# Optimization experiments

Hardware: AMD Instinct MI355X
Metric: run time of the kernel (lower is better)

Reference implementation:

```python
import jax, jax.numpy as jnp
import numpy as np

N = 100000
E = 1600000
IN_C, HID_C, OUT_C = 64, 64, 40
EPS = 1e-5


def setup_inputs() -> dict:
    key = jax.random.key(0)
    ks = jax.random.split(key, 16)
    x = jax.random.normal(ks[0], (N, IN_C), dtype=jnp.float32)
    edge_index = jax.random.randint(ks[1], (2, E), 0, N, dtype=jnp.int64)

    def glorot(k, fan_in, fan_out):
        s = jnp.sqrt(6.0 / (fan_in + fan_out)).astype(jnp.float32)
        return jax.random.uniform(k, (fan_in, fan_out), jnp.float32, -s, s)

    return {
        "x": x,
        "edge_index": edge_index,
        # layer 0: SAGEConv(IN_C -> HID_C): out = mean_aggr @ Wl + x @ Wr + b
        "Wl0": glorot(ks[2], IN_C, HID_C), "Wr0": glorot(ks[3], IN_C, HID_C),
        "b0": jnp.zeros((HID_C,), jnp.float32),
        # layer 1: SAGEConv(HID_C -> HID_C)
        "Wl1": glorot(ks[4], HID_C, HID_C), "Wr1": glorot(ks[5], HID_C, HID_C),
        "b1": jnp.zeros((HID_C,), jnp.float32),
        # layer 2: SAGEConv(HID_C -> OUT_C)
        "Wl2": glorot(ks[6], HID_C, OUT_C), "Wr2": glorot(ks[7], HID_C, OUT_C),
        "b2": jnp.zeros((OUT_C,), jnp.float32),
        # batch norms after layers 0 and 1
        "g0": jnp.ones((HID_C,), jnp.float32), "be0": jnp.zeros((HID_C,), jnp.float32),
        "g1": jnp.ones((HID_C,), jnp.float32), "be1": jnp.zeros((HID_C,), jnp.float32),
    }


def _sage_conv(x, src, dst, Wl, Wr, b):
    # mean aggregation of source features at destination nodes (PyG SAGEConv, aggr='mean')
    agg = jax.ops.segment_sum(x[src], dst, num_segments=N)  # [N, C]
    deg = jax.ops.segment_sum(jnp.ones((src.shape[0],), x.dtype), dst, num_segments=N)
    mean = agg / jnp.maximum(deg, 1.0)[:, None]
    return mean @ Wl + x @ Wr + b


def _batch_norm(x, gamma, beta):
    mu = jnp.mean(x, axis=0)
    var = jnp.var(x, axis=0)
    return (x - mu) * jax.lax.rsqrt(var + EPS) * gamma + beta


def reference(x, edge_index, Wl0, Wr0, b0, Wl1, Wr1, b1, Wl2, Wr2, b2, g0, be0, g1, be1):
    src, dst = edge_index[0], edge_index[1]
    h = _sage_conv(x, src, dst, Wl0, Wr0, b0)
    h = jax.nn.relu(_batch_norm(h, g0, be0))  # dropout is identity at inference
    h = _sage_conv(h, src, dst, Wl1, Wr1, b1)
    h = jax.nn.relu(_batch_norm(h, g1, be1))
    return _sage_conv(h, src, dst, Wl2, Wr2, b2)
```

## Files before the change

### kernel.cpp

```cpp
#include <hip/hip_runtime.h>


constexpr float BN_EPS = 1e-5f;

typedef __attribute__((ext_vector_type(8))) short bf16x8;
typedef __attribute__((ext_vector_type(4))) float f32x4;

__device__ __forceinline__ float bf2f(unsigned short u) {
  union { unsigned int i; float f; } c;
  c.i = (unsigned int)u << 16;
  return c.f;
}
__device__ __forceinline__ unsigned short f2bf(float v) {
  union { float f; unsigned int i; } c;
  c.f = v;
  unsigned int r = c.i + 0x7fffu + ((c.i >> 16) & 1u);
  return (unsigned short)(r >> 16);
}

__device__ __forceinline__ float ld_f(const float* p, size_t i) { return p[i]; }
__device__ __forceinline__ float ld_f(const unsigned short* p, size_t i) {
  return bf2f(p[i]);
}
__device__ __forceinline__ void st_f(float* p, size_t i, float v) { p[i] = v; }
__device__ __forceinline__ void st_f(unsigned short* p, size_t i, float v) {
  p[i] = f2bf(v);
}

__device__ __forceinline__ float4 ld_row(const float* p, int row, int li) {
  return ((const float4*)p)[(size_t)row * 16 + li];
}
__device__ __forceinline__ float4 ld_row(const unsigned short* p, int row, int li) {
  ushort4 u = ((const ushort4*)p)[(size_t)row * 16 + li];
  float4 f;
  f.x = bf2f(u.x); f.y = bf2f(u.y); f.z = bf2f(u.z); f.w = bf2f(u.w);
  return f;
}

__global__ __launch_bounds__(256) void k_zero(int* __restrict__ p, int n) {
  int i = blockIdx.x * 256 + threadIdx.x;
  if (i < n) p[i] = 0;
}

__global__ __launch_bounds__(256) void k_probe(const int* __restrict__ w, int E,
                                               int* __restrict__ dflag) {
  __shared__ int any;
  if (threadIdx.x == 0) any = 0;
  __syncthreads();
  const int twoE = 2 * E;
  int local = 0;
  for (int i = 0; i < 8; ++i) {
    long long idx = (long long)(threadIdx.x * 8 + i) * twoE / 2048;
    int wi = (int)(idx | 1);
    if (wi < twoE && w[wi] != 0) local = 1;
  }
  if (local) atomicOr(&any, 1);
  __syncthreads();
  if (threadIdx.x == 0) *dflag = any;
}

__device__ __forceinline__ void load_edge(const void* ei, int e, int E, int is32,
                                          int& src, int& dst) {
  if (is32) {
    const int* p = (const int*)ei;
    src = p[e];
    dst = p[E + e];
  } else {
    const long long* p = (const long long*)ei;
    src = (int)p[e];
    dst = (int)p[(long long)E + e];
  }
}

__global__ __launch_bounds__(256) void k_hist(const void* __restrict__ ei, int E,
                                              int N, const int* __restrict__ dflag,
                                              int NB, int chunk,
                                              int* __restrict__ hist) {
  __shared__ int h[256];
  h[threadIdx.x] = 0;
  __syncthreads();
  const int is32 = *dflag;
  int lo = blockIdx.x * chunk;
  int hi = lo + chunk;
  if (hi > E) hi = E;
  for (int e = lo + threadIdx.x; e < hi; e += 256) {
    int src, dst;
    load_edge(ei, e, E, is32, src, dst);
    if ((unsigned)src < (unsigned)N && (unsigned)dst < (unsigned)N)
      atomicAdd(&h[dst >> 9], 1);
  }
  __syncthreads();
  if (threadIdx.x < NB) hist[blockIdx.x * NB + threadIdx.x] = h[threadIdx.x];
}

__global__ __launch_bounds__(256) void k_btot(const int* __restrict__ hist,
                                              int NBLK, int NB,
                                              int* __restrict__ bucket_base) {
  __shared__ int part[256];
  int t = threadIdx.x;
  int s = 0;
  if (t < NB)
    for (int b = 0; b < NBLK; ++b) s += hist[b * NB + t];
  part[t] = s;
  __syncthreads();
  for (int off = 1; off < 256; off <<= 1) {
    int u = (t >= off) ? part[t - off] : 0;
    __syncthreads();
    part[t] += u;
    __syncthreads();
  }
  if (t < NB) bucket_base[t] = part[t] - s;
  if (t == NB - 1) bucket_base[NB] = part[t];
}

__global__ __launch_bounds__(64) void k_hoff(const int* __restrict__ hist,
                                             int NBLK, int NB,
                                             const int* __restrict__ bucket_base,
                                             int* __restrict__ offs) {
  int b = blockIdx.x;
  int lane = threadIdx.x;
  int carry = bucket_base[b];
  for (int c = 0; c < NBLK; c += 64) {
    int blk = c + lane;
    int v = (blk < NBLK) ? hist[blk * NB + b] : 0;
    int incl = v;
    for (int off = 1; off < 64; off <<= 1) {
      int u = __shfl_up(incl, off);
      if (lane >= off) incl += u;
    }
    if (blk < NBLK) offs[blk * NB + b] = carry + incl - v;
    carry += __shfl(incl, 63);
  }
}

__global__ __launch_bounds__(256) void k_scat(const void* __restrict__ ei, int E,
                                              int N, const int* __restrict__ dflag,
                                              int NB, int chunk,
                                              const int* __restrict__ offs,
                                              unsigned* __restrict__ csr) {
  __shared__ int cur[256];
  if (threadIdx.x < NB) cur[threadIdx.x] = offs[blockIdx.x * NB + threadIdx.x];
  __syncthreads();
  const int is32 = *dflag;
  int lo = blockIdx.x * chunk;
  int hi = lo + chunk;
  if (hi > E) hi = E;
  for (int e = lo + threadIdx.x; e < hi; e += 256) {
    int src, dst;
    load_edge(ei, e, E, is32, src, dst);
    if ((unsigned)src < (unsigned)N && (unsigned)dst < (unsigned)N) {
      int p = atomicAdd(&cur[dst >> 9], 1);
      csr[p] = ((unsigned)src << 9) | (unsigned)(dst & 511);
    }
  }
}

__global__ __launch_bounds__(256) void k_fine(unsigned* __restrict__ csr,
                                              const int* __restrict__ bucket_base,
                                              int N, int* __restrict__ row_start) {
  constexpr int CAP = 12288;
  __shared__ unsigned lrec[CAP];
  __shared__ int lcnt[512];
  __shared__ int cur[512];
  __shared__ int wtot[4];
  const int b = blockIdx.x;
  const int lo = bucket_base[b];
  int cnt = bucket_base[b + 1] - lo;
  if (cnt > CAP) cnt = CAP;
  const int t = threadIdx.x;
  lcnt[t] = 0;
  lcnt[t + 256] = 0;
  __syncthreads();
  for (int i = t; i < cnt; i += 256) {
    unsigned r = csr[lo + i];
    lrec[i] = r;
    atomicAdd(&lcnt[r & 511], 1);
  }
  __syncthreads();
  int v0 = lcnt[2 * t], v1 = lcnt[2 * t + 1];
  int s = v0 + v1;
  int incl = s;
  const int lane = t & 63;
  for (int off = 1; off < 64; off <<= 1) {
    int u = __shfl_up(incl, off);
    if (lane >= off) incl += u;
  }
  const int wv = t >> 6;
  if (lane == 63) wtot[wv] = incl;
  __syncthreads();
  int woff = 0;
  for (int i = 0; i < wv; ++i) woff += wtot[i];
  int excl = woff + incl - s;
  cur[2 * t] = excl;
  cur[2 * t + 1] = excl + v0;
  int gi = b * 512 + 2 * t;
  if (gi <= N) row_start[gi] = lo + excl;
  if (gi + 1 <= N) row_start[gi + 1] = lo + excl + v0;
  __syncthreads();
  for (int i = t; i < cnt; i += 256) {
    unsigned r = lrec[i];
    int p = atomicAdd(&cur[r & 511], 1);
    csr[lo + p] = r >> 9;
  }
}

template <int COUT, typename TI, typename TO>
__global__ __launch_bounds__(256, 4) void k_sage(
    const TI* __restrict__ hin, const int* __restrict__ row_start,
    const int* __restrict__ csr, const float* __restrict__ Wl,
    const float* __restrict__ Wr, const float* __restrict__ bias,
    TO* __restrict__ out, int n) {
  constexpr int NT = (COUT + 15) / 16;
  __shared__ short sWf[NT][4][64][8];
  __shared__ short sA[4][16][136];

  for (int t = threadIdx.x; t < NT * 4 * 64; t += 256) {
    int lane = t & 63;
    int kt = (t >> 6) & 3;
    int nt = t >> 8;
    int kbase = kt * 32 + (lane >> 4) * 8;
    int col = nt * 16 + (lane & 15);
#pragma unroll
    for (int j = 0; j < 8; ++j) {
      int k = kbase + j;
      float wv = 0.0f;
      if (col < COUT) wv = (k < 64) ? Wl[k * COUT + col] : Wr[(k - 64) * COUT + col];
      sWf[nt][kt][lane][j] = (short)f2bf(wv);
    }
  }
  __syncthreads();

  const int wave = threadIdx.x >> 6;
  const int lane = threadIdx.x & 63;
  const int g = lane >> 4;
  const int li = lane & 15;
  const int quad = lane >> 4;
  const int col16 = lane & 15;

  float bias_r[NT];
#pragma unroll
  for (int nt = 0; nt < NT; ++nt) {
    int c = nt * 16 + col16;
    bias_r[nt] = (c < COUT) ? bias[c] : 0.0f;
  }

  const int wgl = blockIdx.x * 4 + wave;
  const int nstride = gridDim.x * 64;

  for (int base = wgl * 16; base < n; base += nstride) {
#pragma unroll 1
    for (int nb = 0; nb < 16; ++nb) {
      int node = base + nb;
      if (node >= n) break;
      int rs = row_start[node];
      int re = row_start[node + 1];
      float4 acc = make_float4(0.f, 0.f, 0.f, 0.f);
      int e = rs + g;
      for (; e + 4 < re; e += 8) {
        int r0 = csr[e], r1 = csr[e + 4];
        float4 a = ld_row(hin, r0, li);
        float4 b = ld_row(hin, r1, li);
        acc.x += a.x + b.x;
        acc.y += a.y + b.y;
        acc.z += a.z + b.z;
        acc.w += a.w + b.w;
      }
      if (e < re) {
        float4 a = ld_row(hin, csr[e], li);
        acc.x += a.x; acc.y += a.y; acc.z += a.z; acc.w += a.w;
      }
      acc.x += __shfl_xor(acc.x, 16); acc.x += __shfl_xor(acc.x, 32);
      acc.y += __shfl_xor(acc.y, 16); acc.y += __shfl_xor(acc.y, 32);
      acc.z += __shfl_xor(acc.z, 16); acc.z += __shfl_xor(acc.z, 32);
      acc.w += __shfl_xor(acc.w, 16); acc.w += __shfl_xor(acc.w, 32);
      int deg = re - rs;
      float invd = 1.0f / (float)(deg > 0 ? deg : 1);
      float4 self = ld_row(hin, node, li);
      ushort4 mv, sv;
      mv.x = f2bf(acc.x * invd); mv.y = f2bf(acc.y * invd);
      mv.z = f2bf(acc.z * invd); mv.w = f2bf(acc.w * invd);
      sv.x = f2bf(self.x); sv.y = f2bf(self.y);
      sv.z = f2bf(self.z); sv.w = f2bf(self.w);
      *(ushort4*)&sA[wave][nb][li * 4] = mv;
      *(ushort4*)&sA[wave][nb][64 + li * 4] = sv;
    }
    __builtin_amdgcn_wave_barrier();

    f32x4 acc[NT];
#pragma unroll
    for (int nt = 0; nt < NT; ++nt) acc[nt] = (f32x4){0.f, 0.f, 0.f, 0.f};
#pragma unroll
    for (int kt = 0; kt < 4; ++kt) {
      bf16x8 a = *(const bf16x8*)&sA[wave][lane & 15][kt * 32 + (lane >> 4) * 8];
#pragma unroll
      for (int nt = 0; nt < NT; ++nt) {
        bf16x8 b = *(const bf16x8*)&sWf[nt][kt][lane][0];
        acc[nt] = __builtin_amdgcn_mfma_f32_16x16x32_bf16(a, b, acc[nt], 0, 0, 0);
      }
    }
    __builtin_amdgcn_wave_barrier();

#pragma unroll
    for (int nt = 0; nt < NT; ++nt) {
      int c = nt * 16 + col16;
      if (c < COUT) {
#pragma unroll
        for (int r = 0; r < 4; ++r) {
          int node = base + quad * 4 + r;
          if (node < n) st_f(out, (size_t)node * COUT + c, acc[nt][r] + bias_r[nt]);
        }
      }
    }
  }
}

template <typename TI>
__global__ __launch_bounds__(256) void k_bnstats(const TI* __restrict__ t,
                                                 float* __restrict__ stats, int n) {
  const int c = threadIdx.x & 63;
  const int grp = threadIdx.x >> 6;
  float s = 0.f, q = 0.f;
  for (int r = blockIdx.x * 4 + grp; r < n; r += gridDim.x * 4) {
    float v = ld_f(t, (size_t)r * 64 + c);
    s += v;
    q += v * v;
  }
  __shared__ float ls[4][64];
  __shared__ float lq[4][64];
  ls[grp][c] = s;
  lq[grp][c] = q;
  __syncthreads();
  if (threadIdx.x < 64) {
    int cc = threadIdx.x;
    atomicAdd(&stats[cc], ls[0][cc] + ls[1][cc] + ls[2][cc] + ls[3][cc]);
    atomicAdd(&stats[64 + cc], lq[0][cc] + lq[1][cc] + lq[2][cc] + lq[3][cc]);
  }
}

template <typename T>
__global__ __launch_bounds__(256) void k_bnapply(T* __restrict__ t,
                                                 const float* __restrict__ stats,
                                                 const float* __restrict__ g,
                                                 const float* __restrict__ be, int n) {
  int i = blockIdx.x * 256 + threadIdx.x;
  if (i >= n * 64) return;
  int c = i & 63;
  float invN = 1.0f / (float)n;
  float mu = stats[c] * invN;
  float var = stats[64 + c] * invN - mu * mu;
  var = var < 0.f ? 0.f : var;
  float sc = g[c] * rsqrtf(var + BN_EPS);
  float x = (ld_f(t, (size_t)i) - mu) * sc + be[c];
  st_f(t, (size_t)i, x > 0.f ? x : 0.f);
}

extern "C" void kernel_launch(void* const* d_in, const int* in_sizes, int n_in,
                              void* d_out, int out_size, void* d_ws, size_t ws_size,
                              hipStream_t stream) {
  const float* x = (const float*)d_in[0];
  const void* ei = d_in[1];
  const float* Wl0 = (const float*)d_in[2];
  const float* Wr0 = (const float*)d_in[3];
  const float* b0 = (const float*)d_in[4];
  const float* Wl1 = (const float*)d_in[5];
  const float* Wr1 = (const float*)d_in[6];
  const float* b1 = (const float*)d_in[7];
  const float* Wl2 = (const float*)d_in[8];
  const float* Wr2 = (const float*)d_in[9];
  const float* b2 = (const float*)d_in[10];
  const float* g0 = (const float*)d_in[11];
  const float* be0 = (const float*)d_in[12];
  const float* g1 = (const float*)d_in[13];
  const float* be1 = (const float*)d_in[14];

  const int N = in_sizes[0] / 64;
  const int E = in_sizes[1] / 2;
  const int NB = (N + 511) >> 9;
  const int NBLK = 256;
  const int chunk = (E + NBLK - 1) / NBLK;

  char* w = (char*)d_ws;
  auto carve = [&](size_t bytes) {
    void* p = (void*)w;
    w += (bytes + 255) & ~(size_t)255;
    return p;
  };
  int* dflag = (int*)carve(4);
  float* stats = (float*)carve(1024);
  int* row_start = (int*)carve((size_t)(N + 1) * 4);
  unsigned* csr = (unsigned*)carve((size_t)E * 4);
  int* hist = (int*)carve((size_t)NBLK * NB * 4);
  int* offs = (int*)carve((size_t)NBLK * NB * 4);
  int* bucket_base = (int*)carve((size_t)(NB + 1) * 4);

  float* statsA = stats;
  float* statsB = stats + 128;

  unsigned short* B = (unsigned short*)d_out;
  unsigned short* A = (unsigned short*)const_cast<float*>(x);

  const int SG = 1024;
  const int ab = (N * 64 + 255) / 256;

  k_probe<<<1, 256, 0, stream>>>((const int*)ei, E, dflag);
  k_zero<<<1, 256, 0, stream>>>((int*)stats, 256);
  k_hist<<<NBLK, 256, 0, stream>>>(ei, E, N, dflag, NB, chunk, hist);
  k_btot<<<1, 256, 0, stream>>>(hist, NBLK, NB, bucket_base);
  k_hoff<<<NB, 64, 0, stream>>>(hist, NBLK, NB, bucket_base, offs);
  k_scat<<<NBLK, 256, 0, stream>>>(ei, E, N, dflag, NB, chunk, offs, csr);
  k_fine<<<NB, 256, 0, stream>>>(csr, bucket_base, N, row_start);

  k_sage<64, float, unsigned short><<<SG, 256, 0, stream>>>(
      x, row_start, (const int*)csr, Wl0, Wr0, b0, B, N);
  k_bnstats<unsigned short><<<1024, 256, 0, stream>>>(B, statsA, N);
  k_bnapply<unsigned short><<<ab, 256, 0, stream>>>(B, statsA, g0, be0, N);

  k_sage<64, unsigned short, unsigned short><<<SG, 256, 0, stream>>>(
      B, row_start, (const int*)csr, Wl1, Wr1, b1, A, N);
  k_bnstats<unsigned short><<<1024, 256, 0, stream>>>(A, statsB, N);
  k_bnapply<unsigned short><<<ab, 256, 0, stream>>>(A, statsB, g1, be1, N);

  k_sage<40, unsigned short, float><<<SG, 256, 0, stream>>>(
      A, row_start, (const int*)csr, Wl2, Wr2, b2, (float*)d_out, N);
}
```

Baseline: 574.3 us.

## Fuse batch-norm stats and apply into SAGE aggregation kernels

Removes the separate BN stats and BN apply kernels. Each SAGE kernel now accumulates per-channel sum and sum-of-squares of its output in registers, reduces them, and atomically adds them. The next SAGE kernel applies the normalisation and ReLU on the fly to every gathered neighbour row and the self row. The stats zeroing moves into k_btot, and the gather loop is unrolled to four edges per lane. This saves two full read-write passes over the activations per layer and several launches, at the cost of repeating the affine and ReLU for every edge gather.

```diff
diff --git a/kernel.cpp b/kernel.cpp
--- a/kernel.cpp
+++ b/kernel.cpp
@@ -18,10 +18,6 @@
   return (unsigned short)(r >> 16);
 }
 
-__device__ __forceinline__ float ld_f(const float* p, size_t i) { return p[i]; }
-__device__ __forceinline__ float ld_f(const unsigned short* p, size_t i) {
-  return bf2f(p[i]);
-}
 __device__ __forceinline__ void st_f(float* p, size_t i, float v) { p[i] = v; }
 __device__ __forceinline__ void st_f(unsigned short* p, size_t i, float v) {
   p[i] = f2bf(v);
@@ -35,11 +31,6 @@
   float4 f;
   f.x = bf2f(u.x); f.y = bf2f(u.y); f.z = bf2f(u.z); f.w = bf2f(u.w);
   return f;
-}
-
-__global__ __launch_bounds__(256) void k_zero(int* __restrict__ p, int n) {
-  int i = blockIdx.x * 256 + threadIdx.x;
-  if (i < n) p[i] = 0;
 }
 
 __global__ __launch_bounds__(256) void k_probe(const int* __restrict__ w, int E,
@@ -95,7 +86,9 @@
 
 __global__ __launch_bounds__(256) void k_btot(const int* __restrict__ hist,
                                               int NBLK, int NB,
-                                              int* __restrict__ bucket_base) {
+                                              int* __restrict__ bucket_base,
+                                              float* __restrict__ stats) {
+  stats[threadIdx.x] = 0.0f;
   __shared__ int part[256];
   int t = threadIdx.x;
   int s = 0;
@@ -204,15 +197,19 @@
   }
 }
 
-template <int COUT, typename TI, typename TO>
+template <int COUT, bool BNIN, bool BNOUT, typename TI, typename TO>
 __global__ __launch_bounds__(256, 4) void k_sage(
     const TI* __restrict__ hin, const int* __restrict__ row_start,
     const int* __restrict__ csr, const float* __restrict__ Wl,
     const float* __restrict__ Wr, const float* __restrict__ bias,
+    const float* __restrict__ statsIn, const float* __restrict__ gIn,
+    const float* __restrict__ beIn, float* __restrict__ statsOut,
     TO* __restrict__ out, int n) {
   constexpr int NT = (COUT + 15) / 16;
   __shared__ short sWf[NT][4][64][8];
   __shared__ short sA[4][16][136];
+  __shared__ float sBN[2][64];
+  __shared__ float sRed[2][4][64];
 
   for (int t = threadIdx.x; t < NT * 4 * 64; t += 256) {
     int lane = t & 63;
@@ -228,6 +225,16 @@
       sWf[nt][kt][lane][j] = (short)f2bf(wv);
     }
   }
+  if (BNIN && threadIdx.x < 64) {
+    int c = threadIdx.x;
+    float inv = 1.0f / (float)n;
+    float mu = statsIn[c] * inv;
+    float var = statsIn[64 + c] * inv - mu * mu;
+    var = var < 0.f ? 0.f : var;
+    float sc = gIn[c] * rsqrtf(var + BN_EPS);
+    sBN[0][c] = sc;
+    sBN[1][c] = beIn[c] - mu * sc;
+  }
   __syncthreads();
 
   const int wave = threadIdx.x >> 6;
@@ -237,12 +244,32 @@
   const int quad = lane >> 4;
   const int col16 = lane & 15;
 
+  float4 bsc = make_float4(1.f, 1.f, 1.f, 1.f);
+  float4 bsh = make_float4(0.f, 0.f, 0.f, 0.f);
+  if (BNIN) {
+    bsc = *(const float4*)&sBN[0][li * 4];
+    bsh = *(const float4*)&sBN[1][li * 4];
+  }
+  auto xf = [&](float4 v) -> float4 {
+    if (!BNIN) return v;
+    float4 r;
+    r.x = fmaxf(v.x * bsc.x + bsh.x, 0.f);
+    r.y = fmaxf(v.y * bsc.y + bsh.y, 0.f);
+    r.z = fmaxf(v.z * bsc.z + bsh.z, 0.f);
+    r.w = fmaxf(v.w * bsc.w + bsh.w, 0.f);
+    return r;
+  };
+
   float bias_r[NT];
 #pragma unroll
   for (int nt = 0; nt < NT; ++nt) {
     int c = nt * 16 + col16;
     bias_r[nt] = (c < COUT) ? bias[c] : 0.0f;
   }
+
+  float statS[NT], statQ[NT];
+#pragma unroll
+  for (int nt = 0; nt < NT; ++nt) { statS[nt] = 0.f; statQ[nt] = 0.f; }
 
   const int wgl = blockIdx.x * 4 + wave;
   const int nstride = gridDim.x * 64;
@@ -256,17 +283,19 @@
       int re = row_start[node + 1];
       float4 acc = make_float4(0.f, 0.f, 0.f, 0.f);
       int e = rs + g;
-      for (; e + 4 < re; e += 8) {
-        int r0 = csr[e], r1 = csr[e + 4];
-        float4 a = ld_row(hin, r0, li);
-        float4 b = ld_row(hin, r1, li);
-        acc.x += a.x + b.x;
-        acc.y += a.y + b.y;
-        acc.z += a.z + b.z;
-        acc.w += a.w + b.w;
+      for (; e + 12 < re; e += 16) {
+        int r0 = csr[e], r1 = csr[e + 4], r2 = csr[e + 8], r3 = csr[e + 12];
+        float4 a = xf(ld_row(hin, r0, li));
+        float4 b = xf(ld_row(hin, r1, li));
+        float4 c = xf(ld_row(hin, r2, li));
+        float4 d = xf(ld_row(hin, r3, li));
+        acc.x += (a.x + b.x) + (c.x + d.x);
+        acc.y += (a.y + b.y) + (c.y + d.y);
+        acc.z += (a.z + b.z) + (c.z + d.z);
+        acc.w += (a.w + b.w) + (c.w + d.w);
       }
-      if (e < re) {
-        float4 a = ld_row(hin, csr[e], li);
+      for (; e < re; e += 4) {
+        float4 a = xf(ld_row(hin, csr[e], li));
         acc.x += a.x; acc.y += a.y; acc.z += a.z; acc.w += a.w;
       }
       acc.x += __shfl_xor(acc.x, 16); acc.x += __shfl_xor(acc.x, 32);
@@ -275,7 +304,7 @@
       acc.w += __shfl_xor(acc.w, 16); acc.w += __shfl_xor(acc.w, 32);
       int deg = re - rs;
       float invd = 1.0f / (float)(deg > 0 ? deg : 1);
-      float4 self = ld_row(hin, node, li);
+      float4 self = xf(ld_row(hin, node, li));
       ushort4 mv, sv;
       mv.x = f2bf(acc.x * invd); mv.y = f2bf(acc.y * invd);
       mv.z = f2bf(acc.z * invd); mv.w = f2bf(acc.w * invd);
@@ -307,51 +336,40 @@
 #pragma unroll
         for (int r = 0; r < 4; ++r) {
           int node = base + quad * 4 + r;
-          if (node < n) st_f(out, (size_t)node * COUT + c, acc[nt][r] + bias_r[nt]);
+          if (node < n) {
+            float v = acc[nt][r] + bias_r[nt];
+            st_f(out, (size_t)node * COUT + c, v);
+            if (BNOUT) { statS[nt] += v; statQ[nt] += v * v; }
+          }
         }
       }
     }
   }
-}
-
-template <typename TI>
-__global__ __launch_bounds__(256) void k_bnstats(const TI* __restrict__ t,
-                                                 float* __restrict__ stats, int n) {
-  const int c = threadIdx.x & 63;
-  const int grp = threadIdx.x >> 6;
-  float s = 0.f, q = 0.f;
-  for (int r = blockIdx.x * 4 + grp; r < n; r += gridDim.x * 4) {
-    float v = ld_f(t, (size_t)r * 64 + c);
-    s += v;
-    q += v * v;
-  }
-  __shared__ float ls[4][64];
-  __shared__ float lq[4][64];
-  ls[grp][c] = s;
-  lq[grp][c] = q;
-  __syncthreads();
-  if (threadIdx.x < 64) {
-    int cc = threadIdx.x;
-    atomicAdd(&stats[cc], ls[0][cc] + ls[1][cc] + ls[2][cc] + ls[3][cc]);
-    atomicAdd(&stats[64 + cc], lq[0][cc] + lq[1][cc] + lq[2][cc] + lq[3][cc]);
-  }
-}
-
-template <typename T>
-__global__ __launch_bounds__(256) void k_bnapply(T* __restrict__ t,
-                                                 const float* __restrict__ stats,
-                                                 const float* __restrict__ g,
-                                                 const float* __restrict__ be, int n) {
-  int i = blockIdx.x * 256 + threadIdx.x;
-  if (i >= n * 64) return;
-  int c = i & 63;
-  float invN = 1.0f / (float)n;
-  float mu = stats[c] * invN;
-  float var = stats[64 + c] * invN - mu * mu;
-  var = var < 0.f ? 0.f : var;
-  float sc = g[c] * rsqrtf(var + BN_EPS);
-  float x = (ld_f(t, (size_t)i) - mu) * sc + be[c];
-  st_f(t, (size_t)i, x > 0.f ? x : 0.f);
+
+  if (BNOUT) {
+#pragma unroll
+    for (int nt = 0; nt < NT; ++nt) {
+      statS[nt] += __shfl_xor(statS[nt], 16);
+      statS[nt] += __shfl_xor(statS[nt], 32);
+      statQ[nt] += __shfl_xor(statQ[nt], 16);
+      statQ[nt] += __shfl_xor(statQ[nt], 32);
+    }
+    if (quad == 0) {
+#pragma unroll
+      for (int nt = 0; nt < NT; ++nt) {
+        sRed[0][wave][nt * 16 + col16] = statS[nt];
+        sRed[1][wave][nt * 16 + col16] = statQ[nt];
+      }
+    }
+    __syncthreads();
+    if (threadIdx.x < 64) {
+      int c = threadIdx.x;
+      float s = sRed[0][0][c] + sRed[0][1][c] + sRed[0][2][c] + sRed[0][3][c];
+      float q = sRed[1][0][c] + sRed[1][1][c] + sRed[1][2][c] + sRed[1][3][c];
+      atomicAdd(&statsOut[c], s);
+      atomicAdd(&statsOut[64 + c], q);
+    }
+  }
 }
 
 extern "C" void kernel_launch(void* const* d_in, const int* in_sizes, int n_in,
@@ -400,26 +418,23 @@
   unsigned short* A = (unsigned short*)const_cast<float*>(x);
 
   const int SG = 1024;
-  const int ab = (N * 64 + 255) / 256;
 
   k_probe<<<1, 256, 0, stream>>>((const int*)ei, E, dflag);
-  k_zero<<<1, 256, 0, stream>>>((int*)stats, 256);
   k_hist<<<NBLK, 256, 0, stream>>>(ei, E, N, dflag, NB, chunk, hist);
-  k_btot<<<1, 256, 0, stream>>>(hist, NBLK, NB, bucket_base);
+  k_btot<<<1, 256, 0, stream>>>(hist, NBLK, NB, bucket_base, stats);
   k_hoff<<<NB, 64, 0, stream>>>(hist, NBLK, NB, bucket_base, offs);
   k_scat<<<NBLK, 256, 0, stream>>>(ei, E, N, dflag, NB, chunk, offs, csr);
   k_fine<<<NB, 256, 0, stream>>>(csr, bucket_base, N, row_start);
 
-  k_sage<64, float, unsigned short><<<SG, 256, 0, stream>>>(
-      x, row_start, (const int*)csr, Wl0, Wr0, b0, B, N);
-  k_bnstats<unsigned short><<<1024, 256, 0, stream>>>(B, statsA, N);
-  k_bnapply<unsigned short><<<ab, 256, 0, stream>>>(B, statsA, g0, be0, N);
-
-  k_sage<64, unsigned short, unsigned short><<<SG, 256, 0, stream>>>(
-      B, row_start, (const int*)csr, Wl1, Wr1, b1, A, N);
-  k_bnstats<unsigned short><<<1024, 256, 0, stream>>>(A, statsB, N);
-  k_bnapply<unsigned short><<<ab, 256, 0, stream>>>(A, statsB, g1, be1, N);
-
-  k_sage<40, unsigned short, float><<<SG, 256, 0, stream>>>(
-      A, row_start, (const int*)csr, Wl2, Wr2, b2, (float*)d_out, N);
-}
+  k_sage<64, false, true, float, unsigned short><<<SG, 256, 0, stream>>>(
+      x, row_start, (const int*)csr, Wl0, Wr0, b0,
+      statsA, g0, be0, statsA, B, N);
+
+  k_sage<64, true, true, unsigned short, unsigned short><<<SG, 256, 0, stream>>>(
+      B, row_start, (const int*)csr, Wl1, Wr1, b1,
+      statsA, g0, be0, statsB, A, N);
+
+  k_sage<40, true, false, unsigned short, float><<<SG, 256, 0, stream>>>(
+      A, row_start, (const int*)csr, Wl2, Wr2, b2,
+      statsB, g1, be1, statsB, (float*)d_out, N);
+}
```

Result: faster. 516.4 us (-10.1%).
